# Kernel optimization log

Hardware: AMD Instinct MI355X
Metric: run time of the kernel (lower is better)

## Reference

```python
import jax, jax.numpy as jnp
import numpy as np

NUM_VALUES = 1048576   # rows in the source value store
NUM_WEIGHTS = 65536    # unique learned weight matrices (deduplicated)
E = 4194304            # total (neuron, input) edges across the layer
DIN = 8
DOUT = 8


def setup_inputs() -> dict:
    key = jax.random.key(0)
    k1, k2, k3, k4 = jax.random.split(key, 4)
    values = jax.random.normal(k1, (NUM_VALUES, DIN), dtype=jnp.float32)
    weights = jax.random.normal(k2, (NUM_WEIGHTS, DOUT, DIN), dtype=jnp.float32)
    input_idx = jax.random.randint(k3, (E,), 0, NUM_VALUES, dtype=jnp.int32)
    weight_idx = jax.random.randint(k4, (E,), 0, NUM_WEIGHTS, dtype=jnp.int32)
    return {"values": values, "weights": weights,
            "input_idx": input_idx, "weight_idx": weight_idx}


def reference(values, weights, input_idx, weight_idx):
    # self.gather(layer_values): gather activations by precomputed ordinals
    x = jnp.take(values, input_idx, axis=0)          # [E, DIN]
    # self.gather_weights(w): gather (possibly shared) weight matrices
    w = jnp.take(weights, weight_idx, axis=0)        # [E, DOUT, DIN]
    # y = w @ input_values  (per-edge dense matmul)
    y = jnp.einsum('eoi,ei->eo', w, x)               # [E, DOUT]
    return y
```

## Files before the change

### kernel.cpp

```cpp
#include <hip/hip_runtime.h>
#include <hip/hip_bf16.h>
#include <stdint.h>


typedef float          f32x4 __attribute__((ext_vector_type(4)));
typedef unsigned int   u32x4 __attribute__((ext_vector_type(4)));
typedef unsigned short u16x4 __attribute__((ext_vector_type(4)));

__device__ __forceinline__ float bflo(uint32_t u) {
    union { uint32_t u; float f; } c; c.u = u << 16; return c.f;
}
__device__ __forceinline__ float bfhi(uint32_t u) {
    union { uint32_t u; float f; } c; c.u = u & 0xffff0000u; return c.f;
}

__global__ __launch_bounds__(256) void convert_f32_bf16_kernel(
    const f32x4* __restrict__ src,
    u16x4*       __restrict__ dst,
    int n4)
{
    int i = blockIdx.x * blockDim.x + threadIdx.x;
    if (i >= n4) return;
    f32x4 v = src[i];
    u16x4 r;
    r.x = __bfloat16_as_ushort(__float2bfloat16(v.x));
    r.y = __bfloat16_as_ushort(__float2bfloat16(v.y));
    r.z = __bfloat16_as_ushort(__float2bfloat16(v.z));
    r.w = __bfloat16_as_ushort(__float2bfloat16(v.w));
    dst[i] = r;
}

__global__ __launch_bounds__(256) void edge_linear_bf16wv_kernel(
    const uint32_t* __restrict__ vbf,
    const uint32_t* __restrict__ wbf,
    const int*      __restrict__ input_idx,
    const int*      __restrict__ weight_idx,
    float*          __restrict__ out,
    int E)
{
    int gid = blockIdx.x * blockDim.x + threadIdx.x;
    int e = gid >> 3;
    if (e >= E) return;
    int o = gid & 7;

    int iidx = input_idx[e];
    int widx = weight_idx[e];

    const u32x4* xp = (const u32x4*)(vbf + (size_t)iidx * 4u);
    const u32x4* wp = (const u32x4*)(wbf + (size_t)widx * 32u + (uint32_t)o * 4u);

    u32x4 wv = *wp;
    u32x4 xv = *xp;

    float acc = 0.0f;
    acc = fmaf(bflo(wv.x), bflo(xv.x), acc);
    acc = fmaf(bfhi(wv.x), bfhi(xv.x), acc);
    acc = fmaf(bflo(wv.y), bflo(xv.y), acc);
    acc = fmaf(bfhi(wv.y), bfhi(xv.y), acc);
    acc = fmaf(bflo(wv.z), bflo(xv.z), acc);
    acc = fmaf(bfhi(wv.z), bfhi(xv.z), acc);
    acc = fmaf(bflo(wv.w), bflo(xv.w), acc);
    acc = fmaf(bfhi(wv.w), bfhi(xv.w), acc);

    out[gid] = acc;
}

__global__ __launch_bounds__(256) void edge_linear_bf16w_kernel(
    const float*    __restrict__ values,
    const uint32_t* __restrict__ wbf,
    const int*      __restrict__ input_idx,
    const int*      __restrict__ weight_idx,
    float*          __restrict__ out,
    int E)
{
    int gid = blockIdx.x * blockDim.x + threadIdx.x;
    int e = gid >> 3;
    if (e >= E) return;
    int o = gid & 7;
    int iidx = input_idx[e];
    int widx = weight_idx[e];
    const f32x4* xp = (const f32x4*)(values + (size_t)iidx * 8u);
    const u32x4* wp = (const u32x4*)(wbf + (size_t)widx * 32u + (uint32_t)o * 4u);
    u32x4 wv = *wp;
    f32x4 x0 = xp[0];
    f32x4 x1 = xp[1];
    float acc = 0.0f;
    acc = fmaf(bflo(wv.x), x0.x, acc);
    acc = fmaf(bfhi(wv.x), x0.y, acc);
    acc = fmaf(bflo(wv.y), x0.z, acc);
    acc = fmaf(bfhi(wv.y), x0.w, acc);
    acc = fmaf(bflo(wv.z), x1.x, acc);
    acc = fmaf(bfhi(wv.z), x1.y, acc);
    acc = fmaf(bflo(wv.w), x1.z, acc);
    acc = fmaf(bfhi(wv.w), x1.w, acc);
    out[gid] = acc;
}

__global__ __launch_bounds__(256) void edge_linear_f32_kernel(
    const float* __restrict__ values,
    const float* __restrict__ weights,
    const int*   __restrict__ input_idx,
    const int*   __restrict__ weight_idx,
    float*       __restrict__ out,
    int E)
{
    int gid = blockIdx.x * blockDim.x + threadIdx.x;
    int e = gid >> 3;
    if (e >= E) return;
    int o = gid & 7;
    int iidx = input_idx[e];
    int widx = weight_idx[e];
    const float4* xp = (const float4*)(values  + (size_t)iidx * 8u);
    const float4* wp = (const float4*)(weights + (size_t)widx * 64u + (uint32_t)o * 8u);
    float4 x0 = xp[0], x1 = xp[1], w0 = wp[0], w1 = wp[1];
    float acc = 0.0f;
    acc = fmaf(w0.x, x0.x, acc); acc = fmaf(w0.y, x0.y, acc);
    acc = fmaf(w0.z, x0.z, acc); acc = fmaf(w0.w, x0.w, acc);
    acc = fmaf(w1.x, x1.x, acc); acc = fmaf(w1.y, x1.y, acc);
    acc = fmaf(w1.z, x1.z, acc); acc = fmaf(w1.w, x1.w, acc);
    out[gid] = acc;
}

extern "C" void kernel_launch(void* const* d_in, const int* in_sizes, int n_in,
                              void* d_out, int out_size, void* d_ws, size_t ws_size,
                              hipStream_t stream) {
    const float* values     = (const float*)d_in[0];
    const float* weights    = (const float*)d_in[1];
    const int*   input_idx  = (const int*)d_in[2];
    const int*   weight_idx = (const int*)d_in[3];
    float*       out        = (float*)d_out;

    int NV = in_sizes[0];
    int NW = in_sizes[1];
    int E  = in_sizes[2];

    size_t need_w  = (size_t)NW * sizeof(uint16_t);
    size_t v_off   = (need_w + 255u) & ~(size_t)255u;
    size_t need_wv = v_off + (size_t)NV * sizeof(uint16_t);

    long long threads = (long long)E * 8;
    int block = 256;
    int grid = (int)((threads + block - 1) / block);

    if (ws_size >= need_wv) {
        uint16_t* wbf = (uint16_t*)d_ws;
        uint16_t* vbf = (uint16_t*)((char*)d_ws + v_off);
        int wn4 = NW / 4;
        convert_f32_bf16_kernel<<<(wn4 + 255) / 256, 256, 0, stream>>>(
            (const f32x4*)weights, (u16x4*)wbf, wn4);
        int vn4 = NV / 4;
        convert_f32_bf16_kernel<<<(vn4 + 255) / 256, 256, 0, stream>>>(
            (const f32x4*)values, (u16x4*)vbf, vn4);
        edge_linear_bf16wv_kernel<<<grid, block, 0, stream>>>(
            (const uint32_t*)vbf, (const uint32_t*)wbf,
            input_idx, weight_idx, out, E);
    } else if (ws_size >= need_w) {
        int wn4 = NW / 4;
        convert_f32_bf16_kernel<<<(wn4 + 255) / 256, 256, 0, stream>>>(
            (const f32x4*)weights, (u16x4*)d_ws, wn4);
        edge_linear_bf16w_kernel<<<grid, block, 0, stream>>>(
            values, (const uint32_t*)d_ws, input_idx, weight_idx, out, E);
    } else {
        edge_linear_f32_kernel<<<grid, block, 0, stream>>>(
            values, weights, input_idx, weight_idx, out, E);
    }
}
```

Baseline: 319.8 us.

## Bucket-sort edges by input row and stage value rows in LDS

Adds a counting sort (histogram, scan, scatter) that groups edges into 1024 buckets by input row range. Each bucket block converts its contiguous value rows to bf16 once into shared memory and gathers activations from LDS, replacing random global gathers. This trades the random value gathers for several extra passes over the index arrays, an 8-byte-per-edge sorted buffer write and read, and scattered nontemporal output stores.

```diff
diff --git a/kernel.cpp b/kernel.cpp
--- a/kernel.cpp
+++ b/kernel.cpp
@@ -7,17 +7,23 @@
 typedef unsigned int   u32x4 __attribute__((ext_vector_type(4)));
 typedef unsigned short u16x4 __attribute__((ext_vector_type(4)));
 
-__device__ __forceinline__ float bflo(uint32_t u) {
+#define NB  1024
+#define RPB 1024
+
+static __device__ __forceinline__ float bflo(uint32_t u) {
     union { uint32_t u; float f; } c; c.u = u << 16; return c.f;
 }
-__device__ __forceinline__ float bfhi(uint32_t u) {
+static __device__ __forceinline__ float bfhi(uint32_t u) {
     union { uint32_t u; float f; } c; c.u = u & 0xffff0000u; return c.f;
 }
-
-__global__ __launch_bounds__(256) void convert_f32_bf16_kernel(
-    const f32x4* __restrict__ src,
-    u16x4*       __restrict__ dst,
-    int n4)
+static __device__ __forceinline__ uint32_t pack_bf16x2(float lo, float hi) {
+    uint32_t l = __bfloat16_as_ushort(__float2bfloat16(lo));
+    uint32_t h = __bfloat16_as_ushort(__float2bfloat16(hi));
+    return l | (h << 16);
+}
+
+__global__ __launch_bounds__(256) void convert_w_kernel(
+    const f32x4* __restrict__ src, u16x4* __restrict__ dst, int n4)
 {
     int i = blockIdx.x * blockDim.x + threadIdx.x;
     if (i >= n4) return;
@@ -30,6 +36,157 @@
     dst[i] = r;
 }
 
+__global__ __launch_bounds__(NB) void zero_hist_kernel(uint32_t* __restrict__ g)
+{
+    g[threadIdx.x] = 0u;
+}
+
+__global__ __launch_bounds__(256) void hist_kernel(
+    const int* __restrict__ input_idx, uint32_t* __restrict__ ghist,
+    int E, int bshift)
+{
+    __shared__ uint32_t h[NB];
+    for (int i = threadIdx.x; i < NB; i += 256) h[i] = 0u;
+    __syncthreads();
+    int base = blockIdx.x * 8192;
+    #pragma unroll
+    for (int k = 0; k < 32; ++k) {
+        int ei = base + k * 256 + threadIdx.x;
+        if (ei < E) {
+            uint32_t b = ((uint32_t)input_idx[ei]) >> bshift;
+            atomicAdd(&h[b], 1u);
+        }
+    }
+    __syncthreads();
+    for (int i = threadIdx.x; i < NB; i += 256) {
+        uint32_t v = h[i];
+        if (v) atomicAdd(&ghist[i], v);
+    }
+}
+
+__global__ __launch_bounds__(NB) void scan_kernel(
+    const uint32_t* __restrict__ ghist,
+    uint32_t* __restrict__ bucket_base,
+    uint32_t* __restrict__ cursor)
+{
+    __shared__ uint32_t s[NB];
+    int t = threadIdx.x;
+    uint32_t orig = ghist[t];
+    s[t] = orig;
+    __syncthreads();
+    for (int off = 1; off < NB; off <<= 1) {
+        uint32_t v = (t >= off) ? s[t - off] : 0u;
+        __syncthreads();
+        s[t] += v;
+        __syncthreads();
+    }
+    uint32_t excl = s[t] - orig;
+    bucket_base[t] = excl;
+    cursor[t] = excl;
+    if (t == NB - 1) bucket_base[NB] = s[t];
+}
+
+__global__ __launch_bounds__(1024) void scatter_kernel(
+    const int* __restrict__ input_idx,
+    const int* __restrict__ weight_idx,
+    uint32_t*  __restrict__ cursor,
+    uint2*     __restrict__ sorted,
+    int E, int bshift)
+{
+    __shared__ uint32_t h[NB];
+    int t = threadIdx.x;
+    h[t] = 0u;
+    __syncthreads();
+    int base = blockIdx.x * 8192;
+    uint32_t ii[8], wi[8];
+    #pragma unroll
+    for (int k = 0; k < 8; ++k) {
+        int ei = base + k * 1024 + t;
+        if (ei < E) {
+            ii[k] = (uint32_t)input_idx[ei];
+            wi[k] = (uint32_t)weight_idx[ei];
+            atomicAdd(&h[ii[k] >> bshift], 1u);
+        }
+    }
+    __syncthreads();
+    uint32_t cnt = h[t];
+    uint32_t gb = 0u;
+    if (cnt) gb = atomicAdd(&cursor[t], cnt);
+    h[t] = gb;
+    __syncthreads();
+    uint32_t mask = (1u << bshift) - 1u;
+    #pragma unroll
+    for (int k = 0; k < 8; ++k) {
+        int ei = base + k * 1024 + t;
+        if (ei < E) {
+            uint32_t b = ii[k] >> bshift;
+            uint32_t pos = atomicAdd(&h[b], 1u);
+            uint2 rec;
+            rec.x = ((ii[k] & mask) << 16) | wi[k];
+            rec.y = (uint32_t)ei;
+            sorted[pos] = rec;
+        }
+    }
+}
+
+__global__ __launch_bounds__(256) void edge_linear_sorted_kernel(
+    const float*    __restrict__ values,
+    const uint32_t* __restrict__ wbf,
+    const uint2*    __restrict__ sorted,
+    const uint32_t* __restrict__ bucket_base,
+    float*          __restrict__ out,
+    int rows, int bshift)
+{
+    __shared__ u32x4 vlds[RPB];
+    int b = blockIdx.x >> 1;
+    int c = blockIdx.x & 1;
+    int s    = (int)bucket_base[b];
+    int tend = (int)bucket_base[b + 1];
+    int half = (tend - s + 1) >> 1;
+    int lo = s + c * half;
+    int hi = min(tend, lo + half);
+
+    int spb   = 1 << bshift;
+    int rbase = b << bshift;
+    for (int r = threadIdx.x; r < spb; r += 256) {
+        int row = rbase + r;
+        u32x4 v = {0u, 0u, 0u, 0u};
+        if (row < rows) {
+            const f32x4* vp = (const f32x4*)(values + (size_t)row * 8u);
+            f32x4 a0 = vp[0];
+            f32x4 a1 = vp[1];
+            v.x = pack_bf16x2(a0.x, a0.y);
+            v.y = pack_bf16x2(a0.z, a0.w);
+            v.z = pack_bf16x2(a1.x, a1.y);
+            v.w = pack_bf16x2(a1.z, a1.w);
+        }
+        vlds[r] = v;
+    }
+    __syncthreads();
+
+    int g = threadIdx.x >> 3;
+    int o = threadIdx.x & 7;
+
+    for (int p = lo + g; p < hi; p += 32) {
+        uint2 rec = sorted[p];
+        uint32_t local = rec.x >> 16;
+        uint32_t widx  = rec.x & 0xffffu;
+        uint32_t e     = rec.y;
+        u32x4 xv = vlds[local];
+        u32x4 wv = *(const u32x4*)(wbf + (size_t)widx * 32u + (uint32_t)o * 4u);
+        float acc = 0.0f;
+        acc = fmaf(bflo(wv.x), bflo(xv.x), acc);
+        acc = fmaf(bfhi(wv.x), bfhi(xv.x), acc);
+        acc = fmaf(bflo(wv.y), bflo(xv.y), acc);
+        acc = fmaf(bfhi(wv.y), bfhi(xv.y), acc);
+        acc = fmaf(bflo(wv.z), bflo(xv.z), acc);
+        acc = fmaf(bfhi(wv.z), bfhi(xv.z), acc);
+        acc = fmaf(bflo(wv.w), bflo(xv.w), acc);
+        acc = fmaf(bfhi(wv.w), bfhi(xv.w), acc);
+        __builtin_nontemporal_store(acc, &out[(size_t)e * 8u + (uint32_t)o]);
+    }
+}
+
 __global__ __launch_bounds__(256) void edge_linear_bf16wv_kernel(
     const uint32_t* __restrict__ vbf,
     const uint32_t* __restrict__ wbf,
@@ -42,16 +199,12 @@
     int e = gid >> 3;
     if (e >= E) return;
     int o = gid & 7;
-
     int iidx = input_idx[e];
     int widx = weight_idx[e];
-
     const u32x4* xp = (const u32x4*)(vbf + (size_t)iidx * 4u);
     const u32x4* wp = (const u32x4*)(wbf + (size_t)widx * 32u + (uint32_t)o * 4u);
-
     u32x4 wv = *wp;
     u32x4 xv = *xp;
-
     float acc = 0.0f;
     acc = fmaf(bflo(wv.x), bflo(xv.x), acc);
     acc = fmaf(bfhi(wv.x), bfhi(xv.x), acc);
@@ -61,39 +214,21 @@
     acc = fmaf(bfhi(wv.z), bfhi(xv.z), acc);
     acc = fmaf(bflo(wv.w), bflo(xv.w), acc);
     acc = fmaf(bfhi(wv.w), bfhi(xv.w), acc);
-
     out[gid] = acc;
 }
 
-__global__ __launch_bounds__(256) void edge_linear_bf16w_kernel(
-    const float*    __restrict__ values,
-    const uint32_t* __restrict__ wbf,
-    const int*      __restrict__ input_idx,
-    const int*      __restrict__ weight_idx,
-    float*          __restrict__ out,
-    int E)
-{
-    int gid = blockIdx.x * blockDim.x + threadIdx.x;
-    int e = gid >> 3;
-    if (e >= E) return;
-    int o = gid & 7;
-    int iidx = input_idx[e];
-    int widx = weight_idx[e];
-    const f32x4* xp = (const f32x4*)(values + (size_t)iidx * 8u);
-    const u32x4* wp = (const u32x4*)(wbf + (size_t)widx * 32u + (uint32_t)o * 4u);
-    u32x4 wv = *wp;
-    f32x4 x0 = xp[0];
-    f32x4 x1 = xp[1];
-    float acc = 0.0f;
-    acc = fmaf(bflo(wv.x), x0.x, acc);
-    acc = fmaf(bfhi(wv.x), x0.y, acc);
-    acc = fmaf(bflo(wv.y), x0.z, acc);
-    acc = fmaf(bfhi(wv.y), x0.w, acc);
-    acc = fmaf(bflo(wv.z), x1.x, acc);
-    acc = fmaf(bfhi(wv.z), x1.y, acc);
-    acc = fmaf(bflo(wv.w), x1.z, acc);
-    acc = fmaf(bfhi(wv.w), x1.w, acc);
-    out[gid] = acc;
+__global__ __launch_bounds__(256) void convert_v_kernel(
+    const f32x4* __restrict__ src, u16x4* __restrict__ dst, int n4)
+{
+    int i = blockIdx.x * blockDim.x + threadIdx.x;
+    if (i >= n4) return;
+    f32x4 v = src[i];
+    u16x4 r;
+    r.x = __bfloat16_as_ushort(__float2bfloat16(v.x));
+    r.y = __bfloat16_as_ushort(__float2bfloat16(v.y));
+    r.z = __bfloat16_as_ushort(__float2bfloat16(v.z));
+    r.w = __bfloat16_as_ushort(__float2bfloat16(v.w));
+    dst[i] = r;
 }
 
 __global__ __launch_bounds__(256) void edge_linear_f32_kernel(
@@ -134,32 +269,61 @@
     int NW = in_sizes[1];
     int E  = in_sizes[2];
 
+    int rows = NV / 8;
+    int numW = NW / 64;
+
+    auto aln = [](size_t x) { return (x + 255u) & ~(size_t)255u; };
+
+    size_t off_w    = 0;
+    size_t off_sort = aln((size_t)NW * 2u);
+    size_t off_hist = off_sort + aln((size_t)E * 8u);
+    size_t off_base = off_hist + aln((size_t)NB * 4u);
+    size_t off_cur  = off_base + aln((size_t)(NB + 1) * 4u);
+    size_t need_sort = off_cur + aln((size_t)NB * 4u);
+
+    int bshift = 0;
+    while (bshift < 20 && (((uint32_t)(rows - 1)) >> bshift) >= NB) bshift++;
+    bool sortable = (numW <= 65536) && (rows >= 1) && ((1 << bshift) <= RPB);
+
     size_t need_w  = (size_t)NW * sizeof(uint16_t);
-    size_t v_off   = (need_w + 255u) & ~(size_t)255u;
+    size_t v_off   = aln(need_w);
     size_t need_wv = v_off + (size_t)NV * sizeof(uint16_t);
 
     long long threads = (long long)E * 8;
     int block = 256;
     int grid = (int)((threads + block - 1) / block);
 
-    if (ws_size >= need_wv) {
+    if (sortable && ws_size >= need_sort) {
+        uint16_t* wbf    = (uint16_t*)((char*)d_ws + off_w);
+        uint2*    sorted = (uint2*)   ((char*)d_ws + off_sort);
+        uint32_t* ghist  = (uint32_t*)((char*)d_ws + off_hist);
+        uint32_t* bbase  = (uint32_t*)((char*)d_ws + off_base);
+        uint32_t* cursor = (uint32_t*)((char*)d_ws + off_cur);
+
+        int wn4 = NW / 4;
+        convert_w_kernel<<<(wn4 + 255) / 256, 256, 0, stream>>>(
+            (const f32x4*)weights, (u16x4*)wbf, wn4);
+
+        int sblocks = (E + 8191) / 8192;
+        zero_hist_kernel<<<1, NB, 0, stream>>>(ghist);
+        hist_kernel<<<sblocks, 256, 0, stream>>>(input_idx, ghist, E, bshift);
+        scan_kernel<<<1, NB, 0, stream>>>(ghist, bbase, cursor);
+        scatter_kernel<<<sblocks, 1024, 0, stream>>>(
+            input_idx, weight_idx, cursor, sorted, E, bshift);
+
+        edge_linear_sorted_kernel<<<NB * 2, 256, 0, stream>>>(
+            values, (const uint32_t*)wbf, sorted, bbase, out, rows, bshift);
+    } else if (ws_size >= need_wv) {
         uint16_t* wbf = (uint16_t*)d_ws;
         uint16_t* vbf = (uint16_t*)((char*)d_ws + v_off);
-        int wn4 = NW / 4;
-        convert_f32_bf16_kernel<<<(wn4 + 255) / 256, 256, 0, stream>>>(
+        int wn4 = NW / 4, vn4 = NV / 4;
+        convert_w_kernel<<<(wn4 + 255) / 256, 256, 0, stream>>>(
             (const f32x4*)weights, (u16x4*)wbf, wn4);
-        int vn4 = NV / 4;
-        convert_f32_bf16_kernel<<<(vn4 + 255) / 256, 256, 0, stream>>>(
+        convert_v_kernel<<<(vn4 + 255) / 256, 256, 0, stream>>>(
             (const f32x4*)values, (u16x4*)vbf, vn4);
         edge_linear_bf16wv_kernel<<<grid, block, 0, stream>>>(
             (const uint32_t*)vbf, (const uint32_t*)wbf,
             input_idx, weight_idx, out, E);
-    } else if (ws_size >= need_w) {
-        int wn4 = NW / 4;
-        convert_f32_bf16_kernel<<<(wn4 + 255) / 256, 256, 0, stream>>>(
-            (const f32x4*)weights, (u16x4*)d_ws, wn4);
-        edge_linear_bf16w_kernel<<<grid, block, 0, stream>>>(
-            values, (const uint32_t*)d_ws, input_idx, weight_idx, out, E);
     } else {
         edge_linear_f32_kernel<<<grid, block, 0, stream>>>(
             values, weights, input_idx, weight_idx, out, E);
```

Measured after the change: 434.7 us. 1.36x slower.
